# Optimization experiments

Measured on AMD Instinct MI355X. Metric: run time of the kernel, lower is better.

Reference implementation:

```python
import jax, jax.numpy as jnp
import numpy as np

GRID_RES = 64
BOUND = 1.2

def _coords():
    lin = jnp.linspace(-BOUND, BOUND, GRID_RES, dtype=jnp.float32)
    gx, gy, gz = jnp.meshgrid(lin, lin, lin, indexing='ij')
    return jnp.stack([gx, gy, gz], axis=-1).reshape(-1, 3)  # (R^3, 3)

def setup_inputs() -> dict:
    key = jax.random.key(0)
    ks = jax.random.split(key, 9)
    B, D, H = 2, 512, 512
    s_in = 1.0 / np.sqrt(D + 3)
    s_h = 1.0 / np.sqrt(H)
    return {
        'cad_latent': jax.random.normal(ks[0], (B, D), jnp.float32),
        'W0': jax.random.normal(ks[1], (D + 3, H), jnp.float32) * s_in,
        'b0': jax.random.normal(ks[2], (H,), jnp.float32) * s_in,
        'W1': jax.random.normal(ks[3], (H, H), jnp.float32) * s_h,
        'b1': jax.random.normal(ks[4], (H,), jnp.float32) * s_h,
        'W2': jax.random.normal(ks[5], (H, H), jnp.float32) * s_h,
        'b2': jax.random.normal(ks[6], (H,), jnp.float32) * s_h,
        'W3': jax.random.normal(ks[7], (H, 1), jnp.float32) * s_h,
        'b3': jax.random.normal(ks[8], (1,), jnp.float32) * s_h,
    }

def reference(cad_latent, W0, b0, W1, b1, W2, b2, W3, b3):
    B, D = cad_latent.shape
    coords = _coords()  # (P, 3), P = R^3
    # First layer: concat([latent, coords]) @ W0 decomposed to avoid
    # materializing the broadcast-concatenated (B, P, D+3) tensor.
    lat_part = cad_latent @ W0[:D]          # (B, H)
    coord_part = coords @ W0[D:]            # (P, H)
    h = jax.nn.silu(lat_part[:, None, :] + coord_part[None, :, :] + b0)  # (B, P, H)
    h = jax.nn.silu(h @ W1 + b1)
    h = jax.nn.silu(h @ W2 + b2)
    sdf = h @ W3 + b3                       # (B, P, 1)
    return sdf.reshape(B, GRID_RES, GRID_RES, GRID_RES)
```

## Files before the change

### kernel.cpp

```cpp
#include <hip/hip_runtime.h>

#define H 512
#define MTILE 64
#define NBLK 8192
#define STEPC (2.4f / 63.0f)

typedef _Float16 half8 __attribute__((ext_vector_type(8)));
typedef _Float16 half4_t __attribute__((ext_vector_type(4)));
typedef float floatx16 __attribute__((ext_vector_type(16)));
typedef float floatx4 __attribute__((ext_vector_type(4)));
typedef float floatx2 __attribute__((ext_vector_type(2)));

__device__ inline float silu_f(float x) {
    return __fdividef(x, 1.0f + __expf(-x));
}

__global__ void prep_fused(const float* __restrict__ lat, const float* __restrict__ W0,
                           const float* __restrict__ b0,
                           const float* __restrict__ W1, const float* __restrict__ W2,
                           float* __restrict__ latw, _Float16* __restrict__ ws) {
    __shared__ float sl[H];
    if (blockIdx.x < 1024) {
        const int id = blockIdx.x * 512 + threadIdx.x;
        const int l = id >> 18;
        const int rem = id & 0x3FFFF;
        const int k = rem >> 9, n = rem & 511;
        const float w = (l == 0 ? W1 : W2)[rem];
        const int ks = k >> 4, hi = (k >> 3) & 1, e = k & 7;
        const int wv = n >> 6, nt = (n >> 5) & 1, lm = n & 31;
        ws[(size_t)(l * 8 + wv) * 32768 + hi * 16384 + ks * 512 + nt * 256 + lm * 8 + e]
            = (_Float16)w;
    } else {
        const int b = blockIdx.x - 1024;
        const int j = threadIdx.x;
        sl[j] = lat[b * H + j];
        __syncthreads();
        float acc = b0[j];
#pragma unroll 8
        for (int d = 0; d < H; ++d) acc += sl[d] * W0[d * H + j];
        latw[b * H + j] = acc;
    }
}

__global__ __launch_bounds__(512, 4) void mesh_main(
    const float* __restrict__ W0, const float* __restrict__ b1,
    const float* __restrict__ b2, const float* __restrict__ W3,
    const float* __restrict__ b3, const float* __restrict__ latw,
    const _Float16* __restrict__ wsB, float* __restrict__ out) {

    __shared__ _Float16 hbuf2[4096 * 8];
    __shared__ float lwbuf[2 * H];
    __shared__ float partials[8][MTILE];

    const int tid = threadIdx.x;
    const int wave = tid >> 6, lane = tid & 63;
    const int lm = lane & 31, hi = lane >> 5;
    const int uwave = __builtin_amdgcn_readfirstlane(wave);
    const int bi = blockIdx.x;
    const int b = bi >> 12;
    const int p0 = (bi & 4095) << 6;
    const float c0 = -1.2f + (float)(p0 >> 12) * STEPC;
    const float c1 = -1.2f + (float)((p0 >> 6) & 63) * STEPC;

    auto phase_barrier = [&]() {
        __builtin_amdgcn_sched_barrier(0);
        asm volatile("s_waitcnt lgkmcnt(0)" ::: "memory");
        __builtin_amdgcn_s_barrier();
        __builtin_amdgcn_sched_barrier(0);
    };

    const int vWoffB = hi * 32768 + lm * 16;
    const _Float16* hb = hbuf2 + hi * 512 + lm * 8;

    floatx16 acc[2][2];

    auto zero_acc = [&]() {
#pragma unroll
        for (int mb = 0; mb < 2; ++mb)
#pragma unroll
            for (int nt = 0; nt < 2; ++nt)
#pragma unroll
                for (int r = 0; r < 16; ++r) acc[mb][nt][r] = 0.f;
    };

    auto issueW = [&](const _Float16* base, int ks, half8 (&wf)[2]) {
        const _Float16* sp = base + ks * 512;
        asm volatile("global_load_dwordx4 %0, %2, %3\n\t"
                     "global_load_dwordx4 %1, %2, %3 offset:512"
                     : "=v"(wf[0]), "=v"(wf[1])
                     : "v"(vWoffB), "s"(sp)
                     : "memory");
    };

    auto loadA = [&](int ks, half8 (&a)[2]) {
        const _Float16* hp = hb + ks * 1024;
        a[0] = *(const half8*)(hp);
        a[1] = *(const half8*)(hp + 256);
    };

    auto compute = [&](half8 (&wf)[2], half8 (&a)[2]) {
        __builtin_amdgcn_s_setprio(1);
#pragma unroll
        for (int nt = 0; nt < 2; ++nt)
#pragma unroll
            for (int mb = 0; mb < 2; ++mb)
                acc[mb][nt] = __builtin_amdgcn_mfma_f32_32x32x16_f16(wf[nt], a[mb], acc[mb][nt], 0, 0, 0);
        __builtin_amdgcn_s_setprio(0);
    };

    const _Float16* wbase0 = wsB + (size_t)uwave * 32768;
    const _Float16* wbase1 = wsB + (size_t)(8 + uwave) * 32768;

    half8 Wq[3][2];

    auto run_gemm_body = [&](const _Float16* base) {
        half8 Aq[2][2];
        loadA(0, Aq[0]);
        loadA(1, Aq[1]);
#pragma unroll
        for (int ks = 0; ks < 32; ++ks) {
            if (ks <= 29)      asm volatile("s_waitcnt vmcnt(4)" ::: "memory");
            else if (ks == 30) asm volatile("s_waitcnt vmcnt(2)" ::: "memory");
            else               asm volatile("s_waitcnt vmcnt(0)" ::: "memory");
            __builtin_amdgcn_sched_barrier(0);
            compute(Wq[ks % 3], Aq[ks % 2]);
            if (ks + 3 < 32) issueW(base, ks + 3, Wq[ks % 3]);
            if (ks + 2 < 32) loadA(ks + 2, Aq[ks % 2]);
        }
    };

    {
        const int j = tid;
        const float lwv = latw[b * H + j]
                        + c0 * W0[(H + 0) * H + j]
                        + c1 * W0[(H + 1) * H + j];
        floatx2 v;
        v[0] = lwv;
        v[1] = W0[(H + 2) * H + j];
        *(floatx2*)&lwbuf[2 * j] = v;
    }
    phase_barrier();

    {
        const float c2v = -1.2f + (float)lane * STEPC;
#pragma unroll
        for (int s = 0; s < 8; ++s) {
            const int g = wave * 8 + s;
            const floatx4* lp = (const floatx4*)&lwbuf[g * 16];
            half8 hv;
#pragma unroll
            for (int i = 0; i < 4; ++i) {
                const floatx4 pv = lp[i];
                hv[2 * i + 0] = (_Float16)silu_f(pv[0] + c2v * pv[1]);
                hv[2 * i + 1] = (_Float16)silu_f(pv[2] + c2v * pv[3]);
            }
            *(half8*)&hbuf2[(g * 64 + lane) * 8] = hv;
        }
    }
    zero_acc();
    __builtin_amdgcn_sched_barrier(0);
    issueW(wbase0, 0, Wq[0]);
    issueW(wbase0, 1, Wq[1]);
    issueW(wbase0, 2, Wq[2]);
    phase_barrier();

    run_gemm_body(wbase0);
    phase_barrier();

    {
        _Float16* wb = hbuf2 + (wave * 8) * 512 + lm * 8 + hi * 4;
        floatx4 b1v[2][4];
#pragma unroll
        for (int nt = 0; nt < 2; ++nt)
#pragma unroll
            for (int g = 0; g < 4; ++g)
                b1v[nt][g] = *(const floatx4*)&b1[wave * 64 + nt * 32 + g * 8 + hi * 4];
#pragma unroll
        for (int mb = 0; mb < 2; ++mb)
#pragma unroll
            for (int nt = 0; nt < 2; ++nt)
#pragma unroll
                for (int g = 0; g < 4; ++g) {
                    half4_t hv;
#pragma unroll
                    for (int j = 0; j < 4; ++j)
                        hv[j] = (_Float16)silu_f(acc[mb][nt][g * 4 + j] + b1v[nt][g][j]);
                    *(half4_t*)(wb + (nt * 4 + g) * 512 + mb * 256) = hv;
                }
    }
    zero_acc();
    __builtin_amdgcn_sched_barrier(0);
    issueW(wbase1, 0, Wq[0]);
    issueW(wbase1, 1, Wq[1]);
    issueW(wbase1, 2, Wq[2]);
    phase_barrier();

    run_gemm_body(wbase1);

    {
        floatx4 b2v[2][4], w3v[2][4];
#pragma unroll
        for (int nt = 0; nt < 2; ++nt)
#pragma unroll
            for (int g = 0; g < 4; ++g) {
                const int n0 = wave * 64 + nt * 32 + g * 8 + hi * 4;
                b2v[nt][g] = *(const floatx4*)&b2[n0];
                w3v[nt][g] = *(const floatx4*)&W3[n0];
            }
#pragma unroll
        for (int mb = 0; mb < 2; ++mb) {
            float sum = 0.f;
#pragma unroll
            for (int nt = 0; nt < 2; ++nt)
#pragma unroll
                for (int g = 0; g < 4; ++g)
#pragma unroll
                    for (int j = 0; j < 4; ++j)
                        sum += silu_f(acc[mb][nt][g * 4 + j] + b2v[nt][g][j]) * w3v[nt][g][j];
            sum += __shfl_xor(sum, 32);
            if (hi == 0) partials[wave][mb * 32 + lm] = sum;
        }
    }
    phase_barrier();
    if (tid < MTILE) {
        float o = b3[0];
#pragma unroll
        for (int w = 0; w < 8; ++w) o += partials[w][tid];
        out[(size_t)bi * MTILE + tid] = o;
    }
}

extern "C" void kernel_launch(void* const* d_in, const int* in_sizes, int n_in,
                              void* d_out, int out_size, void* d_ws, size_t ws_size,
                              hipStream_t stream) {
    const float* lat = (const float*)d_in[0];
    const float* W0  = (const float*)d_in[1];
    const float* b0  = (const float*)d_in[2];
    const float* W1  = (const float*)d_in[3];
    const float* b1  = (const float*)d_in[4];
    const float* W2  = (const float*)d_in[5];
    const float* b2  = (const float*)d_in[6];
    const float* W3  = (const float*)d_in[7];
    const float* b3  = (const float*)d_in[8];
    float* out = (float*)d_out;

    float* latw = (float*)d_ws;
    _Float16* wsB = (_Float16*)((char*)d_ws + 4096);

    prep_fused<<<1026, 512, 0, stream>>>(lat, W0, b0, W1, W2, latw, wsB);
    mesh_main<<<NBLK, 512, 0, stream>>>(W0, b1, b2, W3, b3, latw, wsB, out);
}
```

Before: 780.3 us.

## Double the per-block point tile to 128 for more weight reuse

Each block now handles 128 grid points instead of 64. Every wave keeps a 4x2 set of MFMA accumulators, so each weight fragment loaded from global memory feeds twice as many MFMAs. This halves the global weight traffic per point and the number of blocks. In exchange it doubles LDS use (about 128KB hbuf) and accumulator registers, and cuts launch bounds occupancy from 4 to 2 blocks per CU, which may expose more latency.

```diff
diff --git a/kernel.cpp b/kernel.cpp
--- a/kernel.cpp
+++ b/kernel.cpp
@@ -1,15 +1,13 @@
 #include <hip/hip_runtime.h>
 
 #define H 512
-#define MTILE 64
-#define NBLK 8192
+#define NBLK 4096
 #define STEPC (2.4f / 63.0f)
 
 typedef _Float16 half8 __attribute__((ext_vector_type(8)));
 typedef _Float16 half4_t __attribute__((ext_vector_type(4)));
 typedef float floatx16 __attribute__((ext_vector_type(16)));
 typedef float floatx4 __attribute__((ext_vector_type(4)));
-typedef float floatx2 __attribute__((ext_vector_type(2)));
 
 __device__ inline float silu_f(float x) {
     return __fdividef(x, 1.0f + __expf(-x));
@@ -42,25 +40,25 @@
     }
 }
 
-__global__ __launch_bounds__(512, 4) void mesh_main(
+__global__ __launch_bounds__(512, 2) void mesh_main(
     const float* __restrict__ W0, const float* __restrict__ b1,
     const float* __restrict__ b2, const float* __restrict__ W3,
     const float* __restrict__ b3, const float* __restrict__ latw,
     const _Float16* __restrict__ wsB, float* __restrict__ out) {
 
-    __shared__ _Float16 hbuf2[4096 * 8];
-    __shared__ float lwbuf[2 * H];
-    __shared__ float partials[8][MTILE];
+    __shared__ _Float16 hbuf2[8192 * 8];
+    __shared__ floatx4 lwq[H];
+    __shared__ float partials[8][128];
 
     const int tid = threadIdx.x;
     const int wave = tid >> 6, lane = tid & 63;
     const int lm = lane & 31, hi = lane >> 5;
     const int uwave = __builtin_amdgcn_readfirstlane(wave);
     const int bi = blockIdx.x;
-    const int b = bi >> 12;
-    const int p0 = (bi & 4095) << 6;
-    const float c0 = -1.2f + (float)(p0 >> 12) * STEPC;
-    const float c1 = -1.2f + (float)((p0 >> 6) & 63) * STEPC;
+    const int b = bi >> 11;
+    const int pi = bi & 2047;
+    const float c0 = -1.2f + (float)(pi >> 5) * STEPC;
+    const float c1 = -1.2f + (float)((pi & 31) << 1) * STEPC;
 
     auto phase_barrier = [&]() {
         __builtin_amdgcn_sched_barrier(0);
@@ -70,13 +68,13 @@
     };
 
     const int vWoffB = hi * 32768 + lm * 16;
-    const _Float16* hb = hbuf2 + hi * 512 + lm * 8;
-
-    floatx16 acc[2][2];
+    const _Float16* hb = hbuf2 + hi * 1024 + lm * 8;
+
+    floatx16 acc[4][2];
 
     auto zero_acc = [&]() {
 #pragma unroll
-        for (int mb = 0; mb < 2; ++mb)
+        for (int mb = 0; mb < 4; ++mb)
 #pragma unroll
             for (int nt = 0; nt < 2; ++nt)
 #pragma unroll
@@ -92,18 +90,19 @@
                      : "memory");
     };
 
-    auto loadA = [&](int ks, half8 (&a)[2]) {
-        const _Float16* hp = hb + ks * 1024;
-        a[0] = *(const half8*)(hp);
-        a[1] = *(const half8*)(hp + 256);
-    };
-
-    auto compute = [&](half8 (&wf)[2], half8 (&a)[2]) {
+    auto loadA = [&](int ks, half8 (&a)[4]) {
+        const _Float16* hp = hb + ks * 2048;
+#pragma unroll
+        for (int mb = 0; mb < 4; ++mb)
+            a[mb] = *(const half8*)(hp + mb * 256);
+    };
+
+    auto compute = [&](half8 (&wf)[2], half8 (&a)[4]) {
         __builtin_amdgcn_s_setprio(1);
 #pragma unroll
         for (int nt = 0; nt < 2; ++nt)
 #pragma unroll
-            for (int mb = 0; mb < 2; ++mb)
+            for (int mb = 0; mb < 4; ++mb)
                 acc[mb][nt] = __builtin_amdgcn_mfma_f32_32x32x16_f16(wf[nt], a[mb], acc[mb][nt], 0, 0, 0);
         __builtin_amdgcn_s_setprio(0);
     };
@@ -114,7 +113,7 @@
     half8 Wq[3][2];
 
     auto run_gemm_body = [&](const _Float16* base) {
-        half8 Aq[2][2];
+        half8 Aq[2][4];
         loadA(0, Aq[0]);
         loadA(1, Aq[1]);
 #pragma unroll
@@ -131,30 +130,32 @@
 
     {
         const int j = tid;
-        const float lwv = latw[b * H + j]
-                        + c0 * W0[(H + 0) * H + j]
-                        + c1 * W0[(H + 1) * H + j];
-        floatx2 v;
-        v[0] = lwv;
-        v[1] = W0[(H + 2) * H + j];
-        *(floatx2*)&lwbuf[2 * j] = v;
-    }
-    phase_barrier();
-
-    {
-        const float c2v = -1.2f + (float)lane * STEPC;
+        floatx4 v;
+        v[0] = latw[b * H + j] + c0 * W0[(H + 0) * H + j];
+        v[1] = W0[(H + 1) * H + j];
+        v[2] = W0[(H + 2) * H + j];
+        v[3] = 0.f;
+        lwq[j] = v;
+    }
+    phase_barrier();
+
+    {
+        const float cz = -1.2f + (float)lane * STEPC;
 #pragma unroll
         for (int s = 0; s < 8; ++s) {
             const int g = wave * 8 + s;
-            const floatx4* lp = (const floatx4*)&lwbuf[g * 16];
-            half8 hv;
-#pragma unroll
-            for (int i = 0; i < 4; ++i) {
-                const floatx4 pv = lp[i];
-                hv[2 * i + 0] = (_Float16)silu_f(pv[0] + c2v * pv[1]);
-                hv[2 * i + 1] = (_Float16)silu_f(pv[2] + c2v * pv[3]);
+            floatx4 pv[8];
+#pragma unroll
+            for (int i = 0; i < 8; ++i) pv[i] = lwq[g * 8 + i];
+#pragma unroll
+            for (int half = 0; half < 2; ++half) {
+                const float cy = c1 + (float)half * STEPC;
+                half8 hv;
+#pragma unroll
+                for (int i = 0; i < 8; ++i)
+                    hv[i] = (_Float16)silu_f(pv[i][0] + cy * pv[i][1] + cz * pv[i][2]);
+                *(half8*)&hbuf2[(g * 128 + half * 64 + lane) * 8] = hv;
             }
-            *(half8*)&hbuf2[(g * 64 + lane) * 8] = hv;
         }
     }
     zero_acc();
@@ -168,24 +169,24 @@
     phase_barrier();
 
     {
-        _Float16* wb = hbuf2 + (wave * 8) * 512 + lm * 8 + hi * 4;
         floatx4 b1v[2][4];
 #pragma unroll
         for (int nt = 0; nt < 2; ++nt)
 #pragma unroll
-            for (int g = 0; g < 4; ++g)
-                b1v[nt][g] = *(const floatx4*)&b1[wave * 64 + nt * 32 + g * 8 + hi * 4];
-#pragma unroll
-        for (int mb = 0; mb < 2; ++mb)
+            for (int g4 = 0; g4 < 4; ++g4)
+                b1v[nt][g4] = *(const floatx4*)&b1[wave * 64 + nt * 32 + g4 * 8 + hi * 4];
+#pragma unroll
+        for (int mb = 0; mb < 4; ++mb)
 #pragma unroll
             for (int nt = 0; nt < 2; ++nt)
 #pragma unroll
-                for (int g = 0; g < 4; ++g) {
+                for (int g4 = 0; g4 < 4; ++g4) {
                     half4_t hv;
 #pragma unroll
                     for (int j = 0; j < 4; ++j)
-                        hv[j] = (_Float16)silu_f(acc[mb][nt][g * 4 + j] + b1v[nt][g][j]);
-                    *(half4_t*)(wb + (nt * 4 + g) * 512 + mb * 256) = hv;
+                        hv[j] = (_Float16)silu_f(acc[mb][nt][g4 * 4 + j] + b1v[nt][g4][j]);
+                    const int gg = wave * 8 + nt * 4 + g4;
+                    *(half4_t*)&hbuf2[(gg * 128 + mb * 32 + lm) * 8 + hi * 4] = hv;
                 }
     }
     zero_acc();
@@ -202,31 +203,31 @@
 #pragma unroll
         for (int nt = 0; nt < 2; ++nt)
 #pragma unroll
-            for (int g = 0; g < 4; ++g) {
-                const int n0 = wave * 64 + nt * 32 + g * 8 + hi * 4;
-                b2v[nt][g] = *(const floatx4*)&b2[n0];
-                w3v[nt][g] = *(const floatx4*)&W3[n0];
+            for (int g4 = 0; g4 < 4; ++g4) {
+                const int n0 = wave * 64 + nt * 32 + g4 * 8 + hi * 4;
+                b2v[nt][g4] = *(const floatx4*)&b2[n0];
+                w3v[nt][g4] = *(const floatx4*)&W3[n0];
             }
 #pragma unroll
-        for (int mb = 0; mb < 2; ++mb) {
+        for (int mb = 0; mb < 4; ++mb) {
             float sum = 0.f;
 #pragma unroll
             for (int nt = 0; nt < 2; ++nt)
 #pragma unroll
-                for (int g = 0; g < 4; ++g)
+                for (int g4 = 0; g4 < 4; ++g4)
 #pragma unroll
                     for (int j = 0; j < 4; ++j)
-                        sum += silu_f(acc[mb][nt][g * 4 + j] + b2v[nt][g][j]) * w3v[nt][g][j];
+                        sum += silu_f(acc[mb][nt][g4 * 4 + j] + b2v[nt][g4][j]) * w3v[nt][g4][j];
             sum += __shfl_xor(sum, 32);
             if (hi == 0) partials[wave][mb * 32 + lm] = sum;
         }
     }
     phase_barrier();
-    if (tid < MTILE) {
+    if (tid < 128) {
         float o = b3[0];
 #pragma unroll
         for (int w = 0; w < 8; ++w) o += partials[w][tid];
-        out[(size_t)bi * MTILE + tid] = o;
+        out[(size_t)bi * 128 + tid] = o;
     }
 }
 
```

New measurement: 780.7 us. No clear change (+0.1%).

## Restructure GEMM pipeline into 4-step superstages with double-buffered W and A

Applied to the files above, without the earlier changes.

The per-k-step triple-buffered weight pipeline becomes 8 superstages of 4 k-steps each. Weight fragments are double-buffered two superstages ahead, and LDS activation fragments are double-buffered one superstage ahead. Each superstage waits once on vmcnt/lgkmcnt and then issues 16 MFMAs under raised priority. The goal is fewer wait points and deeper global-load latency hiding. In exchange, register use roughly doubles, so launch bounds drop from 4 to 2 blocks per CU, lowering occupancy.

```diff
diff --git a/kernel.cpp b/kernel.cpp
--- a/kernel.cpp
+++ b/kernel.cpp
@@ -42,7 +42,7 @@
     }
 }
 
-__global__ __launch_bounds__(512, 4) void mesh_main(
+__global__ __launch_bounds__(512, 2) void mesh_main(
     const float* __restrict__ W0, const float* __restrict__ b1,
     const float* __restrict__ b2, const float* __restrict__ W3,
     const float* __restrict__ b3, const float* __restrict__ latw,
@@ -98,34 +98,46 @@
         a[1] = *(const half8*)(hp + 256);
     };
 
+    auto issueWss = [&](const _Float16* base, int ss, half8 (&Wbuf)[4][2]) {
+#pragma unroll
+        for (int k = 0; k < 4; ++k) issueW(base, ss * 4 + k, Wbuf[k]);
+    };
+    auto issueAss = [&](int ss, half8 (&Abuf)[4][2]) {
+#pragma unroll
+        for (int k = 0; k < 4; ++k) loadA(ss * 4 + k, Abuf[k]);
+    };
+
     auto compute = [&](half8 (&wf)[2], half8 (&a)[2]) {
-        __builtin_amdgcn_s_setprio(1);
 #pragma unroll
         for (int nt = 0; nt < 2; ++nt)
 #pragma unroll
             for (int mb = 0; mb < 2; ++mb)
                 acc[mb][nt] = __builtin_amdgcn_mfma_f32_32x32x16_f16(wf[nt], a[mb], acc[mb][nt], 0, 0, 0);
-        __builtin_amdgcn_s_setprio(0);
     };
 
     const _Float16* wbase0 = wsB + (size_t)uwave * 32768;
     const _Float16* wbase1 = wsB + (size_t)(8 + uwave) * 32768;
 
-    half8 Wq[3][2];
+    half8 Wq[2][4][2];
+    half8 Aq[2][4][2];
 
     auto run_gemm_body = [&](const _Float16* base) {
-        half8 Aq[2][2];
-        loadA(0, Aq[0]);
-        loadA(1, Aq[1]);
-#pragma unroll
-        for (int ks = 0; ks < 32; ++ks) {
-            if (ks <= 29)      asm volatile("s_waitcnt vmcnt(4)" ::: "memory");
-            else if (ks == 30) asm volatile("s_waitcnt vmcnt(2)" ::: "memory");
-            else               asm volatile("s_waitcnt vmcnt(0)" ::: "memory");
+        issueAss(0, Aq[0]);
+#pragma unroll
+        for (int s = 0; s < 8; ++s) {
+            if (s < 7) asm volatile("s_waitcnt vmcnt(8)" ::: "memory");
+            else       asm volatile("s_waitcnt vmcnt(0)" ::: "memory");
+            asm volatile("s_waitcnt lgkmcnt(0)" ::: "memory");
             __builtin_amdgcn_sched_barrier(0);
-            compute(Wq[ks % 3], Aq[ks % 2]);
-            if (ks + 3 < 32) issueW(base, ks + 3, Wq[ks % 3]);
-            if (ks + 2 < 32) loadA(ks + 2, Aq[ks % 2]);
+            if (s + 1 < 8) issueAss(s + 1, Aq[(s + 1) & 1]);
+            __builtin_amdgcn_sched_barrier(0);
+            __builtin_amdgcn_s_setprio(1);
+#pragma unroll
+            for (int k = 0; k < 4; ++k)
+                compute(Wq[s & 1][k], Aq[s & 1][k]);
+            __builtin_amdgcn_s_setprio(0);
+            __builtin_amdgcn_sched_barrier(0);
+            if (s + 2 < 8) issueWss(base, s + 2, Wq[s & 1]);
         }
     };
 
@@ -159,9 +171,8 @@
     }
     zero_acc();
     __builtin_amdgcn_sched_barrier(0);
-    issueW(wbase0, 0, Wq[0]);
-    issueW(wbase0, 1, Wq[1]);
-    issueW(wbase0, 2, Wq[2]);
+    issueWss(wbase0, 0, Wq[0]);
+    issueWss(wbase0, 1, Wq[1]);
     phase_barrier();
 
     run_gemm_body(wbase0);
@@ -190,9 +201,8 @@
     }
     zero_acc();
     __builtin_amdgcn_sched_barrier(0);
-    issueW(wbase1, 0, Wq[0]);
-    issueW(wbase1, 1, Wq[1]);
-    issueW(wbase1, 2, Wq[2]);
+    issueWss(wbase1, 0, Wq[0]);
+    issueWss(wbase1, 1, Wq[1]);
     phase_barrier();
 
     run_gemm_body(wbase1);
```

After: 824.5 us. 5.7% more time.
